# Kernel optimization log

Hardware: AMD Instinct MI355X
Metric: run time of the kernel (lower is better)

The kernel has to match this reference:

```python
import jax, jax.numpy as jnp
import numpy as np

B, T, I, H, C = 8192, 784, 1, 30, 10


def setup_inputs() -> dict:
    key = jax.random.key(0)
    ks = jax.random.split(key, 7)
    s_ih = 1.0 / np.sqrt(H)
    return {
        "x": jax.random.normal(ks[0], (B, T, I), dtype=jnp.float32),
        "W_ih": jax.random.uniform(ks[1], (H, I), jnp.float32, -s_ih, s_ih),
        "W_hh": jax.random.uniform(ks[2], (H, H), jnp.float32, -s_ih, s_ih),
        "b_ih": jax.random.uniform(ks[3], (H,), jnp.float32, -s_ih, s_ih),
        "b_hh": jax.random.uniform(ks[4], (H,), jnp.float32, -s_ih, s_ih),
        "W_fc": jax.random.uniform(ks[5], (C, H), jnp.float32, -s_ih, s_ih),
        "b_fc": jax.random.uniform(ks[6], (C,), jnp.float32, -s_ih, s_ih),
    }


def reference(x, W_ih, W_hh, b_ih, b_hh, W_fc, b_fc):
    # x: [B, T, I] -> scan over time. h_t = tanh(x_t W_ih^T + b_ih + h W_hh^T + b_hh)
    xs = jnp.swapaxes(x, 0, 1)  # [T, B, I]
    h0 = jnp.zeros((x.shape[0], W_hh.shape[0]), dtype=x.dtype)
    bias = b_ih + b_hh  # [H]

    def step(h, xt):
        h_new = jnp.tanh(xt @ W_ih.T + h @ W_hh.T + bias)
        return h_new, None

    hT, _ = jax.lax.scan(step, h0, xs)  # hT: [B, H] == out[:, -1, :]
    return hT @ W_fc.T + b_fc  # [B, C]
```

## Files before the change

kernel.cpp:

```cpp
#include <hip/hip_runtime.h>


#define BB 8192
#define TT 784
#define HH 30
#define CC 10

typedef __attribute__((ext_vector_type(8))) short  bf16x8;
typedef __attribute__((ext_vector_type(4))) float  f32x4;
typedef __attribute__((ext_vector_type(4))) unsigned uint4v;

#if __has_builtin(__builtin_amdgcn_exp2f)
#define EXP2(v) __builtin_amdgcn_exp2f(v)
#else
#define EXP2(v) __expf((v) * 0.69314718055994531f)
#endif

#define SCL 2.8853900817779268f

__device__ __forceinline__ float tanh_e2(float s) {
    return 1.0f - 2.0f * __builtin_amdgcn_rcpf(EXP2(s) + 1.0f);
}

#define BPAIR(p0, p1, hp, lp) do {                                          \
    asm("v_cvt_pk_bf16_f32 %0, %1, %2" : "=v"(hp) : "v"(p0), "v"(p1));      \
    const float _h0 = __uint_as_float((hp) << 16);                          \
    const float _h1 = __uint_as_float((hp) & 0xffff0000u);                  \
    const float _l0 = (p0) - _h0;                                           \
    const float _l1 = (p1) - _h1;                                           \
    asm("v_cvt_pk_bf16_f32 %0, %1, %2" : "=v"(lp) : "v"(_l0), "v"(_l1));    \
} while (0)

__global__ __launch_bounds__(128)
__attribute__((amdgpu_waves_per_eu(1, 1)))
void rnn_scan_kernel(const float* __restrict__ x,
                     const float* __restrict__ W_ih,
                     const float* __restrict__ W_hh,
                     const float* __restrict__ b_ih,
                     const float* __restrict__ b_hh,
                     const float* __restrict__ W_fc,
                     const float* __restrict__ b_fc,
                     float* __restrict__ out) {
    __shared__ unsigned long long Ehi[2][64][2];
    __shared__ unsigned long long Elo[2][64][2];
    __shared__ float hfc[16][33];

    const int tid  = threadIdx.x;
    const int wv   = tid >> 6;
    const int lane = tid & 63;
    const int n    = lane & 15;
    const int g    = lane >> 4;
    const int b    = blockIdx.x * 16 + n;

    const int rr = 8 * (n >> 2) + (n & 3) + 4 * wv;
    unsigned ah[4], al[4];
#pragma unroll
    for (int d = 0; d < 4; ++d) {
        const int k0 = 8 * g + 2 * d, k1 = k0 + 1;
        const float wa = (rr < HH && k0 < HH) ? SCL * W_hh[rr * HH + k0] : 0.f;
        const float wb = (rr < HH && k1 < HH) ? SCL * W_hh[rr * HH + k1] : 0.f;
        const unsigned ua = __float_as_uint(wa), ub = __float_as_uint(wb);
        ah[d] = (ub & 0xffff0000u) | (ua >> 16);
        const float la = wa - __uint_as_float(ua & 0xffff0000u);
        const float lb = wb - __uint_as_float(ub & 0xffff0000u);
        al[d] = (__float_as_uint(lb) & 0xffff0000u) | (__float_as_uint(la) >> 16);
    }
    bf16x8 Ah = __builtin_bit_cast(bf16x8, (uint4v){ah[0], ah[1], ah[2], ah[3]});
    bf16x8 Al = __builtin_bit_cast(bf16x8, (uint4v){al[0], al[1], al[2], al[3]});
    asm volatile("" : "+v"(Ah), "+v"(Al));

    float bias[4], wih[4];
#pragma unroll
    for (int r = 0; r < 4; ++r) {
        const int q = 8 * g + 4 * wv + r;
        bias[r] = (q < HH) ? SCL * (b_ih[q] + b_hh[q]) : 0.f;
        wih[r]  = (q < HH) ? SCL * W_ih[q] : 0.f;
        asm volatile("" : "+v"(bias[r]), "+v"(wih[r]));
    }

    float h0 = 0.f, h1 = 0.f, h2 = 0.f, h3 = 0.f;

    const float* xp = x + (size_t)b * TT;
    const int NQ = TT / 4;
    float4 xq = *(const float4*)xp;
    float4 xn = *(const float4*)(xp + 4);

    for (int qq = 0; qq < NQ; ++qq) {
        const float4 xf = (qq + 2 < NQ) ? *(const float4*)(xp + (qq + 2) * 4)
                                        : make_float4(0.f, 0.f, 0.f, 0.f);
#pragma unroll
        for (int u = 0; u < 4; ++u) {
            const float xt = (u == 0) ? xq.x : (u == 1) ? xq.y
                           : (u == 2) ? xq.z : xq.w;
            const int buf = u & 1;
            unsigned hp0, hp1, lp0, lp1;
            BPAIR(h0, h1, hp0, lp0);
            BPAIR(h2, h3, hp1, lp1);
            Ehi[buf][lane][wv] = (unsigned long long)hp0 |
                                 ((unsigned long long)hp1 << 32);
            Elo[buf][lane][wv] = (unsigned long long)lp0 |
                                 ((unsigned long long)lp1 << 32);
            f32x4 acc = { fmaf(xt, wih[0], bias[0]), fmaf(xt, wih[1], bias[1]),
                          fmaf(xt, wih[2], bias[2]), fmaf(xt, wih[3], bias[3]) };
            __syncthreads();
            const uint4v bhu = *(const uint4v*)&Ehi[buf][lane][0];
            const uint4v blu = *(const uint4v*)&Elo[buf][lane][0];
            const bf16x8 Bh = __builtin_bit_cast(bf16x8, bhu);
            const bf16x8 Bl = __builtin_bit_cast(bf16x8, blu);
            const f32x4 zed = {0.f, 0.f, 0.f, 0.f};
            acc = __builtin_amdgcn_mfma_f32_16x16x32_bf16(Ah, Bh, acc, 0, 0, 0);
            f32x4 qv = __builtin_amdgcn_mfma_f32_16x16x32_bf16(Ah, Bl, zed, 0, 0, 0);
            qv = __builtin_amdgcn_mfma_f32_16x16x32_bf16(Al, Bh, qv, 0, 0, 0);
            const f32x4 s = acc + qv;
            h0 = tanh_e2(s[0]); h1 = tanh_e2(s[1]);
            h2 = tanh_e2(s[2]); h3 = tanh_e2(s[3]);
        }
        xq = xn;
        xn = xf;
    }

    hfc[n][8 * g + 4 * wv + 0] = h0;
    hfc[n][8 * g + 4 * wv + 1] = h1;
    hfc[n][8 * g + 4 * wv + 2] = h2;
    hfc[n][8 * g + 4 * wv + 3] = h3;
    __syncthreads();
    if (wv == 0) {
#pragma unroll
        for (int j = 0; j < 3; ++j) {
            const int c = g + 4 * j;
            if (c < CC) {
                float acc = b_fc[c];
#pragma unroll
                for (int k = 0; k < HH; ++k)
                    acc = fmaf(W_fc[c * HH + k], hfc[n][k], acc);
                out[(size_t)b * CC + c] = acc;
            }
        }
    }
}

extern "C" void kernel_launch(void* const* d_in, const int* in_sizes, int n_in,
                              void* d_out, int out_size, void* d_ws, size_t ws_size,
                              hipStream_t stream) {
    const float* x    = (const float*)d_in[0];
    const float* W_ih = (const float*)d_in[1];
    const float* W_hh = (const float*)d_in[2];
    const float* b_ih = (const float*)d_in[3];
    const float* b_hh = (const float*)d_in[4];
    const float* W_fc = (const float*)d_in[5];
    const float* b_fc = (const float*)d_in[6];

    hipLaunchKernelGGL(rnn_scan_kernel,
                       dim3(BB / 16), dim3(128), 0, stream,
                       x, W_ih, W_hh, b_ih, b_hh, W_fc, b_fc,
                       (float*)d_out);
}
```

Baseline: 273.6 us.

## Split recurrent MFMA into local and remote halves to overlap barrier latency

Each wave now feeds its own freshly computed h values into the MFMAs directly from registers before the barrier. Only the other wave's half of h is read from LDS after the barrier and added with a second set of MFMAs. The LDS layout is merged into a single uint4 buffer holding hi and lo parts. This hides part of the MFMA latency behind the synchronisation on the serial recurrence, but doubles the MFMA count per step (six instead of three) and adds more vector adds on the critical path.

```diff
diff --git a/kernel.cpp b/kernel.cpp
--- a/kernel.cpp
+++ b/kernel.cpp
@@ -31,6 +31,8 @@
     asm("v_cvt_pk_bf16_f32 %0, %1, %2" : "=v"(lp) : "v"(_l0), "v"(_l1));    \
 } while (0)
 
+#define MFMA(A, B, C) __builtin_amdgcn_mfma_f32_16x16x32_bf16((A), (B), (C), 0, 0, 0)
+
 __global__ __launch_bounds__(128)
 __attribute__((amdgpu_waves_per_eu(1, 1)))
 void rnn_scan_kernel(const float* __restrict__ x,
@@ -41,8 +43,7 @@
                      const float* __restrict__ W_fc,
                      const float* __restrict__ b_fc,
                      float* __restrict__ out) {
-    __shared__ unsigned long long Ehi[2][64][2];
-    __shared__ unsigned long long Elo[2][64][2];
+    __shared__ uint4v E[2][2][64];
     __shared__ float hfc[16][33];
 
     const int tid  = threadIdx.x;
@@ -92,26 +93,40 @@
         for (int u = 0; u < 4; ++u) {
             const float xt = (u == 0) ? xq.x : (u == 1) ? xq.y
                            : (u == 2) ? xq.z : xq.w;
-            const int buf = u & 1;
+            const int p = u & 1;
+
             unsigned hp0, hp1, lp0, lp1;
             BPAIR(h0, h1, hp0, lp0);
             BPAIR(h2, h3, hp1, lp1);
-            Ehi[buf][lane][wv] = (unsigned long long)hp0 |
-                                 ((unsigned long long)hp1 << 32);
-            Elo[buf][lane][wv] = (unsigned long long)lp0 |
-                                 ((unsigned long long)lp1 << 32);
+            E[p][wv][lane] = (uint4v){hp0, hp1, lp0, lp1};
+
+            uint4v bh, bl;
+            if (wv == 0) { bh = (uint4v){hp0, hp1, 0, 0}; bl = (uint4v){lp0, lp1, 0, 0}; }
+            else         { bh = (uint4v){0, 0, hp0, hp1}; bl = (uint4v){0, 0, lp0, lp1}; }
+            const bf16x8 Bh = __builtin_bit_cast(bf16x8, bh);
+            const bf16x8 Bl = __builtin_bit_cast(bf16x8, bl);
+
             f32x4 acc = { fmaf(xt, wih[0], bias[0]), fmaf(xt, wih[1], bias[1]),
                           fmaf(xt, wih[2], bias[2]), fmaf(xt, wih[3], bias[3]) };
+            const f32x4 zed = {0.f, 0.f, 0.f, 0.f};
+            f32x4 P0 = MFMA(Ah, Bh, acc);
+            f32x4 Q0 = MFMA(Ah, Bl, zed);
+            Q0 = MFMA(Al, Bh, Q0);
+
             __syncthreads();
-            const uint4v bhu = *(const uint4v*)&Ehi[buf][lane][0];
-            const uint4v blu = *(const uint4v*)&Elo[buf][lane][0];
-            const bf16x8 Bh = __builtin_bit_cast(bf16x8, bhu);
-            const bf16x8 Bl = __builtin_bit_cast(bf16x8, blu);
-            const f32x4 zed = {0.f, 0.f, 0.f, 0.f};
-            acc = __builtin_amdgcn_mfma_f32_16x16x32_bf16(Ah, Bh, acc, 0, 0, 0);
-            f32x4 qv = __builtin_amdgcn_mfma_f32_16x16x32_bf16(Ah, Bl, zed, 0, 0, 0);
-            qv = __builtin_amdgcn_mfma_f32_16x16x32_bf16(Al, Bh, qv, 0, 0, 0);
-            const f32x4 s = acc + qv;
+            const uint4v rv = E[p][wv ^ 1][lane];
+            const unsigned r0 = rv[0], r1 = rv[1], r2 = rv[2], r3 = rv[3];
+            uint4v ch, cl;
+            if (wv == 0) { ch = (uint4v){0, 0, r0, r1}; cl = (uint4v){0, 0, r2, r3}; }
+            else         { ch = (uint4v){r0, r1, 0, 0}; cl = (uint4v){r2, r3, 0, 0}; }
+            const bf16x8 Ch = __builtin_bit_cast(bf16x8, ch);
+            const bf16x8 Cl = __builtin_bit_cast(bf16x8, cl);
+
+            const f32x4 d1 = MFMA(Ah, Ch, P0);
+            const f32x4 d2 = MFMA(Ah, Cl, Q0);
+            const f32x4 d3 = MFMA(Al, Ch, zed);
+            const f32x4 s  = (d1 + d2) + d3;
+
             h0 = tanh_e2(s[0]); h1 = tanh_e2(s[1]);
             h2 = tanh_e2(s[2]); h3 = tanh_e2(s[3]);
         }
```

Result: slower. 301.4 us (+10.2%).

## Interleave two independent batch tiles per block to hide recurrent step latency

Applied to the files above, without the earlier changes.

Each block now processes 32 sequences as two independent 16-wide chains that share one barrier per timestep, and the grid is halved. The interleaving gives the scheduler independent MFMA and tanh work to overlap the latency of the serial recurrence. The low-part correction MFMAs are also made independent rather than chained. The trade is fewer blocks per CU and more registers and LDS per block.

```diff
diff --git a/kernel.cpp b/kernel.cpp
--- a/kernel.cpp
+++ b/kernel.cpp
@@ -31,6 +31,8 @@
     asm("v_cvt_pk_bf16_f32 %0, %1, %2" : "=v"(lp) : "v"(_l0), "v"(_l1));    \
 } while (0)
 
+#define MFMA(A, B, C) __builtin_amdgcn_mfma_f32_16x16x32_bf16((A), (B), (C), 0, 0, 0)
+
 __global__ __launch_bounds__(128)
 __attribute__((amdgpu_waves_per_eu(1, 1)))
 void rnn_scan_kernel(const float* __restrict__ x,
@@ -41,16 +43,17 @@
                      const float* __restrict__ W_fc,
                      const float* __restrict__ b_fc,
                      float* __restrict__ out) {
-    __shared__ unsigned long long Ehi[2][64][2];
-    __shared__ unsigned long long Elo[2][64][2];
-    __shared__ float hfc[16][33];
+    __shared__ unsigned long long Ehi[2][2][64][2];
+    __shared__ unsigned long long Elo[2][2][64][2];
+    __shared__ float hfc[32][33];
 
     const int tid  = threadIdx.x;
     const int wv   = tid >> 6;
     const int lane = tid & 63;
     const int n    = lane & 15;
     const int g    = lane >> 4;
-    const int b    = blockIdx.x * 16 + n;
+    const int bA   = blockIdx.x * 32 + n;
+    const int bB   = bA + 16;
 
     const int rr = 8 * (n >> 2) + (n & 3) + 4 * wv;
     unsigned ah[4], al[4];
@@ -78,53 +81,92 @@
         asm volatile("" : "+v"(bias[r]), "+v"(wih[r]));
     }
 
-    float h0 = 0.f, h1 = 0.f, h2 = 0.f, h3 = 0.f;
+    float hA0 = 0.f, hA1 = 0.f, hA2 = 0.f, hA3 = 0.f;
+    float hB0 = 0.f, hB1 = 0.f, hB2 = 0.f, hB3 = 0.f;
 
-    const float* xp = x + (size_t)b * TT;
+    const float* xpA = x + (size_t)bA * TT;
+    const float* xpB = x + (size_t)bB * TT;
     const int NQ = TT / 4;
-    float4 xq = *(const float4*)xp;
-    float4 xn = *(const float4*)(xp + 4);
+    float4 xqA = *(const float4*)xpA;
+    float4 xnA = *(const float4*)(xpA + 4);
+    float4 xqB = *(const float4*)xpB;
+    float4 xnB = *(const float4*)(xpB + 4);
 
     for (int qq = 0; qq < NQ; ++qq) {
-        const float4 xf = (qq + 2 < NQ) ? *(const float4*)(xp + (qq + 2) * 4)
-                                        : make_float4(0.f, 0.f, 0.f, 0.f);
+        const bool more = (qq + 2 < NQ);
+        const float4 xfA = more ? *(const float4*)(xpA + (qq + 2) * 4)
+                                : make_float4(0.f, 0.f, 0.f, 0.f);
+        const float4 xfB = more ? *(const float4*)(xpB + (qq + 2) * 4)
+                                : make_float4(0.f, 0.f, 0.f, 0.f);
 #pragma unroll
         for (int u = 0; u < 4; ++u) {
-            const float xt = (u == 0) ? xq.x : (u == 1) ? xq.y
-                           : (u == 2) ? xq.z : xq.w;
-            const int buf = u & 1;
+            const float xtA = (u == 0) ? xqA.x : (u == 1) ? xqA.y
+                            : (u == 2) ? xqA.z : xqA.w;
+            const float xtB = (u == 0) ? xqB.x : (u == 1) ? xqB.y
+                            : (u == 2) ? xqB.z : xqB.w;
+            const int p = u & 1;
+
             unsigned hp0, hp1, lp0, lp1;
-            BPAIR(h0, h1, hp0, lp0);
-            BPAIR(h2, h3, hp1, lp1);
-            Ehi[buf][lane][wv] = (unsigned long long)hp0 |
-                                 ((unsigned long long)hp1 << 32);
-            Elo[buf][lane][wv] = (unsigned long long)lp0 |
-                                 ((unsigned long long)lp1 << 32);
-            f32x4 acc = { fmaf(xt, wih[0], bias[0]), fmaf(xt, wih[1], bias[1]),
-                          fmaf(xt, wih[2], bias[2]), fmaf(xt, wih[3], bias[3]) };
+            BPAIR(hA0, hA1, hp0, lp0);
+            BPAIR(hA2, hA3, hp1, lp1);
+            Ehi[p][0][lane][wv] = (unsigned long long)hp0 |
+                                  ((unsigned long long)hp1 << 32);
+            Elo[p][0][lane][wv] = (unsigned long long)lp0 |
+                                  ((unsigned long long)lp1 << 32);
+            unsigned hq0, hq1, lq0, lq1;
+            BPAIR(hB0, hB1, hq0, lq0);
+            BPAIR(hB2, hB3, hq1, lq1);
+            Ehi[p][1][lane][wv] = (unsigned long long)hq0 |
+                                  ((unsigned long long)hq1 << 32);
+            Elo[p][1][lane][wv] = (unsigned long long)lq0 |
+                                  ((unsigned long long)lq1 << 32);
+
+            f32x4 accA = { fmaf(xtA, wih[0], bias[0]), fmaf(xtA, wih[1], bias[1]),
+                           fmaf(xtA, wih[2], bias[2]), fmaf(xtA, wih[3], bias[3]) };
+            f32x4 accB = { fmaf(xtB, wih[0], bias[0]), fmaf(xtB, wih[1], bias[1]),
+                           fmaf(xtB, wih[2], bias[2]), fmaf(xtB, wih[3], bias[3]) };
+
             __syncthreads();
-            const uint4v bhu = *(const uint4v*)&Ehi[buf][lane][0];
-            const uint4v blu = *(const uint4v*)&Elo[buf][lane][0];
-            const bf16x8 Bh = __builtin_bit_cast(bf16x8, bhu);
-            const bf16x8 Bl = __builtin_bit_cast(bf16x8, blu);
+            const uint4v bhA = *(const uint4v*)&Ehi[p][0][lane][0];
+            const uint4v blA = *(const uint4v*)&Elo[p][0][lane][0];
+            const uint4v bhB = *(const uint4v*)&Ehi[p][1][lane][0];
+            const uint4v blB = *(const uint4v*)&Elo[p][1][lane][0];
+            const bf16x8 BhA = __builtin_bit_cast(bf16x8, bhA);
+            const bf16x8 BlA = __builtin_bit_cast(bf16x8, blA);
+            const bf16x8 BhB = __builtin_bit_cast(bf16x8, bhB);
+            const bf16x8 BlB = __builtin_bit_cast(bf16x8, blB);
+
             const f32x4 zed = {0.f, 0.f, 0.f, 0.f};
-            acc = __builtin_amdgcn_mfma_f32_16x16x32_bf16(Ah, Bh, acc, 0, 0, 0);
-            f32x4 qv = __builtin_amdgcn_mfma_f32_16x16x32_bf16(Ah, Bl, zed, 0, 0, 0);
-            qv = __builtin_amdgcn_mfma_f32_16x16x32_bf16(Al, Bh, qv, 0, 0, 0);
-            const f32x4 s = acc + qv;
-            h0 = tanh_e2(s[0]); h1 = tanh_e2(s[1]);
-            h2 = tanh_e2(s[2]); h3 = tanh_e2(s[3]);
+            accA = MFMA(Ah, BhA, accA);
+            f32x4 q1A = MFMA(Ah, BlA, zed);
+            f32x4 q2A = MFMA(Al, BhA, zed);
+            accB = MFMA(Ah, BhB, accB);
+            f32x4 q1B = MFMA(Ah, BlB, zed);
+            f32x4 q2B = MFMA(Al, BhB, zed);
+            const f32x4 sA = (accA + q1A) + q2A;
+            const f32x4 sB = (accB + q1B) + q2B;
+
+            hA0 = tanh_e2(sA[0]); hA1 = tanh_e2(sA[1]);
+            hA2 = tanh_e2(sA[2]); hA3 = tanh_e2(sA[3]);
+            hB0 = tanh_e2(sB[0]); hB1 = tanh_e2(sB[1]);
+            hB2 = tanh_e2(sB[2]); hB3 = tanh_e2(sB[3]);
         }
-        xq = xn;
-        xn = xf;
+        xqA = xnA; xnA = xfA;
+        xqB = xnB; xnB = xfB;
     }
 
-    hfc[n][8 * g + 4 * wv + 0] = h0;
-    hfc[n][8 * g + 4 * wv + 1] = h1;
-    hfc[n][8 * g + 4 * wv + 2] = h2;
-    hfc[n][8 * g + 4 * wv + 3] = h3;
+    hfc[n     ][8 * g + 4 * wv + 0] = hA0;
+    hfc[n     ][8 * g + 4 * wv + 1] = hA1;
+    hfc[n     ][8 * g + 4 * wv + 2] = hA2;
+    hfc[n     ][8 * g + 4 * wv + 3] = hA3;
+    hfc[16 + n][8 * g + 4 * wv + 0] = hB0;
+    hfc[16 + n][8 * g + 4 * wv + 1] = hB1;
+    hfc[16 + n][8 * g + 4 * wv + 2] = hB2;
+    hfc[16 + n][8 * g + 4 * wv + 3] = hB3;
     __syncthreads();
-    if (wv == 0) {
+    {
+        const int brow = wv * 16 + n;
+        const int bout = blockIdx.x * 32 + brow;
 #pragma unroll
         for (int j = 0; j < 3; ++j) {
             const int c = g + 4 * j;
@@ -132,8 +174,8 @@
                 float acc = b_fc[c];
 #pragma unroll
                 for (int k = 0; k < HH; ++k)
-                    acc = fmaf(W_fc[c * HH + k], hfc[n][k], acc);
-                out[(size_t)b * CC + c] = acc;
+                    acc = fmaf(W_fc[c * HH + k], hfc[brow][k], acc);
+                out[(size_t)bout * CC + c] = acc;
             }
         }
     }
@@ -151,7 +193,7 @@
     const float* b_fc = (const float*)d_in[6];
 
     hipLaunchKernelGGL(rnn_scan_kernel,
-                       dim3(BB / 16), dim3(128), 0, stream,
+                       dim3(BB / 32), dim3(128), 0, stream,
                        x, W_ih, W_hh, b_ih, b_hh, W_fc, b_fc,
                        (float*)d_out);
 }
```

New measurement: 374.0 us. 36.7% more time.
